# Performance work log

Hardware: AMD Instinct MI355X
Metric: run time of the kernel (lower is better)

## Reference

```python
import jax, jax.numpy as jnp
import numpy as np

NUM_HEADS = 12
ACT_BITS = 8
W_BITS = 8
# I-BERT integer softmax constants (2nd-order polynomial approx of exp on (-ln2, 0])
EXP_COEF = (0.35815147, 0.96963238, 1.0)
LN2 = 0.6931471805599453
N_EXP = 30  # max number of ln2 shifts


def ste_round(x):
    # straight-through round
    return x + jax.lax.stop_gradient(jnp.round(x) - x)


def fq_act(x, bits=ACT_BITS):
    """Per-tensor asymmetric uint fake-quant (QAct). Returns (dequant, scale)."""
    mn = jax.lax.stop_gradient(jnp.min(x))
    mx = jax.lax.stop_gradient(jnp.max(x))
    qmax = 2.0 ** bits - 1.0
    scale = jnp.maximum((mx - mn) / qmax, 1e-8)
    zero = jnp.round(-mn / scale)
    q = jnp.clip(ste_round(x / scale) + zero, 0.0, qmax)
    return (q - zero) * scale, scale


def fq_weight(w, bits=W_BITS):
    """Per-output-channel symmetric int fake-quant (QuantLinear weight)."""
    amax = jax.lax.stop_gradient(jnp.max(jnp.abs(w), axis=1, keepdims=True))
    qmax = 2.0 ** (bits - 1) - 1.0
    scale = jnp.maximum(amax / qmax, 1e-8)
    q = jnp.clip(ste_round(w / scale), -qmax - 1.0, qmax)
    return q * scale


def int_softmax(x, scale):
    """I-BERT style integer softmax; `scale` is the quant scale of x."""
    a, b, c = EXP_COEF
    x_int = ste_round(x / scale)
    x_int = x_int - jnp.max(x_int, axis=-1, keepdims=True)  # <= 0
    x0_int = jnp.floor(-LN2 / scale)                         # negative integer
    x_int = jnp.maximum(x_int, N_EXP * x0_int)
    qexp = jnp.floor(x_int / x0_int)                         # >= 0 integer
    r = x_int - x0_int * qexp                                # residual in (x0_int, 0]
    b_int = jnp.floor(b / a / scale)
    c_int = jnp.floor(c / a / (scale * scale))
    p_int = r * (r + b_int) + c_int                          # int polynomial exp(r)
    e = p_int * jnp.exp2(-qexp) * (a * scale * scale)        # exp(x) approx
    return e / jnp.sum(e, axis=-1, keepdims=True)


def setup_inputs() -> dict:
    key = jax.random.key(0)
    ks = jax.random.split(key, 5)
    B, N, C = 64, 197, 768
    x = jax.random.normal(ks[0], (B, N, C), dtype=jnp.float32)
    w_qkv = jax.random.normal(ks[1], (3 * C, C), dtype=jnp.float32) * 0.02
    b_qkv = jax.random.normal(ks[2], (3 * C,), dtype=jnp.float32) * 0.02
    w_proj = jax.random.normal(ks[3], (C, C), dtype=jnp.float32) * 0.02
    b_proj = jax.random.normal(ks[4], (C,), dtype=jnp.float32) * 0.02
    return {"x": x, "w_qkv": w_qkv, "b_qkv": b_qkv, "w_proj": w_proj, "b_proj": b_proj}


def reference(x, w_qkv, b_qkv, w_proj, b_proj):
    B, N, C = x.shape
    H = NUM_HEADS
    D = C // H
    attn_scale = D ** -0.5

    # QuantLinear qkv: fake-quant weight, GEMM, fake-quant output
    qkv = jnp.einsum('bnc,oc->bno', x, fq_weight(w_qkv)) + b_qkv
    qkv, _ = fq_act(qkv)

    q, _ = fq_act(qkv[:, :, :C])          # attn_q_out
    k, _ = fq_act(qkv[:, :, C:2 * C])     # attn_k_out
    v, _ = fq_act(qkv[:, :, 2 * C:])      # attn_v_input

    q = q.reshape(B, N, H, D).transpose(0, 2, 1, 3)  # bhnd
    k = k.reshape(B, N, H, D).transpose(0, 2, 1, 3)
    v = v.reshape(B, N, H, D).transpose(0, 2, 1, 3)

    attn = jnp.einsum('bhnd,bhmd->bhnm', q, k) * attn_scale
    attn, kv_scale = fq_act(attn)          # attn_kv_out, provides scale to intSoft
    attn = int_softmax(attn, kv_scale)     # QuantIntSoft

    out = jnp.einsum('bhnm,bhmd->bhnd', attn, v)
    out = out.transpose(0, 2, 1, 3).reshape(B, N, C)
    out, _ = fq_act(out)                   # attn_v_out

    out = jnp.einsum('bnc,oc->bno', out, fq_weight(w_proj)) + b_proj
    out, _ = fq_act(out)                   # attn_proj output quant
    return out
```

## Files before the change

### kernel.cpp

```cpp
#include <hip/hip_runtime.h>


#define NB 64
#define NN 197
#define NC 768
#define NH 12
#define ND 64
#define NO3 2304
#define NBH (NB*NH)
#define NM (NB*NN)

typedef unsigned int u32;
typedef unsigned short u16;
typedef unsigned long long u64;
typedef short bf16x8 __attribute__((ext_vector_type(8)));
typedef float f32x4 __attribute__((ext_vector_type(4)));

__device__ __forceinline__ u32 fenc(float f){
  u32 u = __float_as_uint(f);
  return (u & 0x80000000u) ? ~u : (u | 0x80000000u);
}
__device__ __forceinline__ float fdec(u32 e){
  return (e & 0x80000000u) ? __uint_as_float(e ^ 0x80000000u) : __uint_as_float(~e);
}
__device__ __forceinline__ float wmin(float v){
#pragma unroll
  for (int o=32;o>0;o>>=1) v = fminf(v, __shfl_xor(v,o,64));
  return v;
}
__device__ __forceinline__ float wmax(float v){
#pragma unroll
  for (int o=32;o>0;o>>=1) v = fmaxf(v, __shfl_xor(v,o,64));
  return v;
}
__device__ __forceinline__ float fqdq(float x, float s, float z){
  float q = rintf(x/s) + z;
  q = fminf(fmaxf(q, 0.f), 255.f);
  return (q - z) * s;
}
__device__ __forceinline__ u16 tobf(float f){
  u32 u = __float_as_uint(f);
  return (u16)((u + 0x7fffu + ((u >> 16) & 1u)) >> 16);
}
__device__ __forceinline__ float frombf(u16 u){
  return __uint_as_float(((u32)u) << 16);
}

__device__ __forceinline__ void qkv_scales(const u32* slots, float* s2, float* z2,
                                           float* s1o, float* z1o){
  float mnr0=fdec(slots[0]), mxr0=fdec(slots[1]);
  float mnr1=fdec(slots[2]), mxr1=fdec(slots[3]);
  float mnr2=fdec(slots[4]), mxr2=fdec(slots[5]);
  float mn1 = fminf(mnr0, fminf(mnr1, mnr2));
  float mx1 = fmaxf(mxr0, fmaxf(mxr1, mxr2));
  float s1 = fmaxf((mx1-mn1)/255.0f, 1e-8f);
  float z1 = rintf(-mn1/s1);
  float a0 = fqdq(mnr0,s1,z1), b0 = fqdq(mxr0,s1,z1);
  float a1 = fqdq(mnr1,s1,z1), b1 = fqdq(mxr1,s1,z1);
  float a2 = fqdq(mnr2,s1,z1), b2 = fqdq(mxr2,s1,z1);
  s2[0] = fmaxf((b0-a0)/255.0f,1e-8f); z2[0] = rintf(-a0/s2[0]);
  s2[1] = fmaxf((b1-a1)/255.0f,1e-8f); z2[1] = rintf(-a1/s2[1]);
  s2[2] = fmaxf((b2-a2)/255.0f,1e-8f); z2[2] = rintf(-a2/s2[2]);
  *s1o = s1; *z1o = z1;
}

__global__ void k_init(u32* slots){
  int t = threadIdx.x;
  if (t < 12) slots[t] = (t & 1) ? 0u : 0xFFFFFFFFu;
}

__global__ __launch_bounds__(256) void k_wquant(const float* __restrict__ wqkv,
    const float* __restrict__ wproj, u16* __restrict__ B1, float* __restrict__ s1,
    u16* __restrict__ B2, float* __restrict__ s2){
  int row = blockIdx.x;
  const float* src; u16* dst; float* sd;
  if (row < NO3){ src = wqkv + (size_t)row*NC; dst = B1 + (size_t)row*NC; sd = s1 + row; }
  else { int r2 = row - NO3; src = wproj + (size_t)r2*NC; dst = B2 + (size_t)r2*NC; sd = s2 + r2; }
  int t = threadIdx.x;
  float w0 = src[t], w1 = src[t+256], w2 = src[t+512];
  float am = fmaxf(fabsf(w0), fmaxf(fabsf(w1), fabsf(w2)));
  __shared__ float red[4];
  am = wmax(am);
  if ((t&63)==0) red[t>>6] = am;
  __syncthreads();
  am = fmaxf(fmaxf(red[0],red[1]), fmaxf(red[2],red[3]));
  float s = fmaxf(am / 127.0f, 1e-8f);
  dst[t]     = tobf(fminf(fmaxf(rintf(w0/s), -128.f), 127.f));
  dst[t+256] = tobf(fminf(fmaxf(rintf(w1/s), -128.f), 127.f));
  dst[t+512] = tobf(fminf(fmaxf(rintf(w2/s), -128.f), 127.f));
  if (t==0) *sd = s;
}

template<int MODE>
__global__ __launch_bounds__(256) void k_mfma_gemm(const float* __restrict__ A,
    const u16* __restrict__ Bw, const float* __restrict__ sw,
    const float* __restrict__ bias, float* __restrict__ C, int K, int O,
    const u32* __restrict__ qslot, u32* oslot)
{
  __shared__ u16 Ah[128*40];
  __shared__ u16 Al[(MODE==0) ? 128*40 : 8];
  __shared__ u16 Bs[128*40];
  __shared__ float redn[4], redx[4];

  int tid = threadIdx.x;
  int l = tid & 63, w = tid >> 6;
  long m0 = (long)blockIdx.y * 128;
  long o0 = (long)blockIdx.x * 128;
  int srow = tid >> 1;
  int scol = (tid & 1) << 4;
  bool arow_ok = (m0 + srow) < NM;
  const float* Ap = A + (arow_ok ? (m0 + srow) : 0) * (long)K + scol;
  const u16*  Bp = Bw + (o0 + srow) * (long)K + scol;

  float sA = 1.f, zA = 0.f;
  if constexpr (MODE==1){
    float mn = fdec(qslot[0]), mx = fdec(qslot[1]);
    sA = fmaxf((mx-mn)/255.0f, 1e-8f);
    zA = rintf(-mn/sA);
  }

  int wm = (w>>1)*64, wn = (w&1)*64;
  int fr = l & 15;
  int fc = (l>>4)*8;

  f32x4 acc[4][4];
#pragma unroll
  for (int mi=0;mi<4;mi++)
#pragma unroll
    for (int ni=0;ni<4;ni++)
#pragma unroll
      for (int j=0;j<4;j++) acc[mi][ni][j] = 0.f;

  for (int k0=0; k0<K; k0+=32){
    float4 av0, av1, av2, av3;
    if (arow_ok){
      av0 = *(const float4*)(Ap + k0);
      av1 = *(const float4*)(Ap + k0 + 4);
      av2 = *(const float4*)(Ap + k0 + 8);
      av3 = *(const float4*)(Ap + k0 + 12);
    } else {
      av0 = av1 = av2 = av3 = make_float4(0.f,0.f,0.f,0.f);
    }
    uint4 bv0 = *(const uint4*)(Bp + k0);
    uint4 bv1 = *(const uint4*)(Bp + k0 + 8);

    float xs[16];
    *(float4*)&xs[0] = av0; *(float4*)&xs[4]  = av1;
    *(float4*)&xs[8] = av2; *(float4*)&xs[12] = av3;
    bf16x8 h0, h1, lo0, lo1;
    if constexpr (MODE==0){
#pragma unroll
      for (int j=0;j<8;j++){
        u16 h = tobf(xs[j]);
        h0[j]  = (short)h;
        lo0[j] = (short)tobf(xs[j] - frombf(h));
      }
#pragma unroll
      for (int j=0;j<8;j++){
        u16 h = tobf(xs[8+j]);
        h1[j]  = (short)h;
        lo1[j] = (short)tobf(xs[8+j] - frombf(h));
      }
    } else {
#pragma unroll
      for (int j=0;j<16;j++){
        float q = fminf(fmaxf(rintf(xs[j]/sA)+zA, 0.f), 255.f) - zA;
        if (j<8) h0[j] = (short)tobf(q); else h1[j-8] = (short)tobf(q);
      }
    }

    __syncthreads();
    *(bf16x8*)&Ah[srow*40 + scol]     = h0;
    *(bf16x8*)&Ah[srow*40 + scol + 8] = h1;
    if constexpr (MODE==0){
      *(bf16x8*)&Al[srow*40 + scol]     = lo0;
      *(bf16x8*)&Al[srow*40 + scol + 8] = lo1;
    }
    *(bf16x8*)&Bs[srow*40 + scol]     = *(bf16x8*)&bv0;
    *(bf16x8*)&Bs[srow*40 + scol + 8] = *(bf16x8*)&bv1;
    __syncthreads();

    bf16x8 bfr[4];
#pragma unroll
    for (int ni=0;ni<4;ni++)
      bfr[ni] = *(const bf16x8*)&Bs[(wn + ni*16 + fr)*40 + fc];
#pragma unroll
    for (int mi=0;mi<4;mi++){
      bf16x8 ah = *(const bf16x8*)&Ah[(wm + mi*16 + fr)*40 + fc];
#pragma unroll
      for (int ni=0;ni<4;ni++)
        acc[mi][ni] = __builtin_amdgcn_mfma_f32_16x16x32_bf16(ah, bfr[ni], acc[mi][ni], 0, 0, 0);
    }
    if constexpr (MODE==0){
#pragma unroll
      for (int mi=0;mi<4;mi++){
        bf16x8 al = *(const bf16x8*)&Al[(wm + mi*16 + fr)*40 + fc];
#pragma unroll
        for (int ni=0;ni<4;ni++)
          acc[mi][ni] = __builtin_amdgcn_mfma_f32_16x16x32_bf16(al, bfr[ni], acc[mi][ni], 0, 0, 0);
      }
    }
  }

  float cmn = 3.4e38f, cmx = -3.4e38f;
#pragma unroll
  for (int ni=0;ni<4;ni++){
    long col = o0 + wn + ni*16 + fr;
    float sc = sw[col];
    if constexpr (MODE==1) sc *= sA;
    float bb = bias[col];
#pragma unroll
    for (int mi=0;mi<4;mi++){
      long row0 = m0 + wm + mi*16 + (l>>4)*4;
#pragma unroll
      for (int j=0;j<4;j++){
        long rr = row0 + j;
        if (rr < NM){
          float v = acc[mi][ni][j] * sc + bb;
          C[rr*(long)O + col] = v;
          cmn = fminf(cmn, v); cmx = fmaxf(cmx, v);
        }
      }
    }
  }
  cmn = wmin(cmn); cmx = wmax(cmx);
  if (l==0){ redn[w] = cmn; redx[w] = cmx; }
  __syncthreads();
  if (tid==0){
    float mn = fminf(fminf(redn[0],redn[1]), fminf(redn[2],redn[3]));
    float mx = fmaxf(fmaxf(redx[0],redx[1]), fmaxf(redx[2],redx[3]));
    int sb = (MODE==0) ? 2*(int)(blockIdx.x/6) : 0;
    atomicMin(&oslot[sb],   fenc(mn));
    atomicMax(&oslot[sb+1], fenc(mx));
  }
}

__global__ __launch_bounds__(256) void k_transcode(const float* __restrict__ qkv,
    u16* __restrict__ codes, const u32* __restrict__ slots){
  float s2[3], z2[3], s1g, z1g;
  qkv_scales(slots, s2, z2, &s1g, &z1g);
  const u32 total = 3u*NBH*NN*16u;
  for (u32 i4 = blockIdx.x*256u + threadIdx.x; i4 < total; i4 += gridDim.x*256u){
    u32 d4 = i4 & 15u;
    u32 t1 = i4 >> 4;
    u32 n  = t1 % NN;
    u32 t2 = t1 / NN;
    u32 bh = t2 % NBH;
    u32 sl = t2 / NBH;
    u32 b = bh / NH, h = bh % NH;
    float4 v = *(const float4*)(qkv + ((size_t)b*NN + n)*NO3 + sl*NC + h*ND + d4*4u);
    float ss = s2[sl], zz = z2[sl];
    u64 c0 = (u64)tobf(fminf(fmaxf(rintf(fqdq(v.x,s1g,z1g)/ss)+zz,0.f),255.f) - zz);
    u64 c1 = (u64)tobf(fminf(fmaxf(rintf(fqdq(v.y,s1g,z1g)/ss)+zz,0.f),255.f) - zz);
    u64 c2 = (u64)tobf(fminf(fmaxf(rintf(fqdq(v.z,s1g,z1g)/ss)+zz,0.f),255.f) - zz);
    u64 c3 = (u64)tobf(fminf(fmaxf(rintf(fqdq(v.w,s1g,z1g)/ss)+zz,0.f),255.f) - zz);
    *(u64*)(codes + ((size_t)sl*NBH*NN + (size_t)bh*NN + n)*ND + d4*4u) =
        c0 | (c1<<16) | (c2<<32) | (c3<<48);
  }
}

template<int PASS>
__global__ __launch_bounds__(256) void k_attn(const u16* __restrict__ codes,
    float* __restrict__ rowmax, u32* slots, float* __restrict__ outp){
  __shared__ u16 Ks[64*72];
  __shared__ u16 Vt[(PASS==2)?64*72:8];
  __shared__ u16 EsH[(PASS==2)?64*72:8];
  __shared__ u16 EsL[(PASS==2)?64*72:8];
  __shared__ float redn[4], redx[4];

  const u16* qc = codes;
  const u16* kc = codes + (size_t)NBH*NN*ND;
  const u16* vc = codes + 2*(size_t)NBH*NN*ND;

  float s2[3], z2[3], s1g, z1g;
  qkv_scales(slots, s2, z2, &s1g, &z1g);
  float ss = 0.125f * s2[0] * s2[1];
  float sv = s2[2];

  float s=1.f, z=0.f, x0=-1.f, bint=0.f, cint=0.f, as2=0.f, x030=0.f;
  if constexpr (PASS==2){
    float mnA = fdec(slots[6]), mxA = fdec(slots[7]);
    s = fmaxf((mxA-mnA)/255.0f, 1e-8f);
    z = rintf(-mnA/s);
    x0 = floorf(-0.6931471805599453f / s);
    bint = floorf((float)(0.96963238/0.35815147) / s);
    cint = floorf((float)(1.0/0.35815147) / (s*s));
    as2 = (0.35815147f*s)*s;
    x030 = 30.f*x0;
  }

  int tid = threadIdx.x;
  int l = tid & 63, w = tid >> 6;
  int bh = blockIdx.y, nt = blockIdx.x;
  int lr = l & 15, lk = l >> 4;

  int qrow = nt*64 + w*16 + lr;
  bf16x8 aq0 = {}, aq1 = {};
  if (qrow < NN){
    const u16* qp = qc + ((size_t)bh*NN + qrow)*ND + lk*8;
    aq0 = *(const bf16x8*)qp;
    aq1 = *(const bf16x8*)(qp + 32);
  }

  int qr[4];
#pragma unroll
  for (int j=0;j<4;j++) qr[j] = nt*64 + w*16 + lk*4 + j;

  float rcode[4] = {0.f,0.f,0.f,0.f};
  if constexpr (PASS==2){
#pragma unroll
    for (int j=0;j<4;j++)
      if (qr[j] < NN)
        rcode[j] = fminf(fmaxf(rintf(rowmax[(size_t)bh*NN + qr[j]]/s)+z,0.f),255.f);
  }

  float gmn = 3.4e38f, gmx = -3.4e38f;
  float rmx[4] = {-3.4e38f,-3.4e38f,-3.4e38f,-3.4e38f};
  float den[4] = {0.f,0.f,0.f,0.f};
  f32x4 num[4];
#pragma unroll
  for (int dt=0;dt<4;dt++)
#pragma unroll
    for (int j=0;j<4;j++) num[dt][j] = 0.f;

  for (int mt=0; mt<4; mt++){
    __syncthreads();
#pragma unroll
    for (int rep=0; rep<2; rep++){
      int task = tid + rep*256;
      int row = task >> 3, dc = task & 7;
      int grow = mt*64 + row;
      bf16x8 kv8 = {};
      if (grow < NN) kv8 = *(const bf16x8*)(kc + ((size_t)bh*NN + grow)*ND + dc*8);
      *(bf16x8*)&Ks[row*72 + dc*8] = kv8;
      if constexpr (PASS==2){
        bf16x8 vv8 = {};
        if (grow < NN) vv8 = *(const bf16x8*)(vc + ((size_t)bh*NN + grow)*ND + dc*8);
#pragma unroll
        for (int jj=0;jj<8;jj++) Vt[(dc*8+jj)*72 + row] = (u16)vv8[jj];
      }
    }
    __syncthreads();

    f32x4 sca[4];
#pragma unroll
    for (int ct=0;ct<4;ct++)
#pragma unroll
      for (int j=0;j<4;j++) sca[ct][j] = 0.f;
#pragma unroll
    for (int ct=0;ct<4;ct++){
      bf16x8 bk0 = *(const bf16x8*)&Ks[(ct*16 + lr)*72 + lk*8];
      bf16x8 bk1 = *(const bf16x8*)&Ks[(ct*16 + lr)*72 + 32 + lk*8];
      sca[ct] = __builtin_amdgcn_mfma_f32_16x16x32_bf16(aq0, bk0, sca[ct], 0,0,0);
      sca[ct] = __builtin_amdgcn_mfma_f32_16x16x32_bf16(aq1, bk1, sca[ct], 0,0,0);
    }

    if constexpr (PASS==1){
#pragma unroll
      for (int ct=0;ct<4;ct++){
        int m = mt*64 + ct*16 + lr;
        bool mv = m < NN;
#pragma unroll
        for (int j=0;j<4;j++){
          float sc = sca[ct][j] * ss;
          if (mv && qr[j] < NN){
            gmn = fminf(gmn, sc); gmx = fmaxf(gmx, sc);
            rmx[j] = fmaxf(rmx[j], sc);
          }
        }
      }
    } else {
#pragma unroll
      for (int ct=0;ct<4;ct++){
        int m = mt*64 + ct*16 + lr;
        bool mv = m < NN;
#pragma unroll
        for (int j=0;j<4;j++){
          float e = 0.f;
          if (mv && qr[j] < NN){
            float sc = sca[ct][j] * ss;
            float code = fminf(fmaxf(rintf(sc/s)+z, 0.f), 255.f);
            float xx = fmaxf(code - rcode[j], x030);
            float qe = floorf(xx / x0);
            float rr = xx - x0*qe;
            float p = rr*(rr + bint) + cint;
            e = scalbnf(p, -(int)qe) * as2;
            den[j] += e;
          }
          u16 eh = tobf(e);
          int ea = (w*16 + lk*4 + j)*72 + ct*16 + lr;
          EsH[ea] = eh;
          EsL[ea] = tobf(e - frombf(eh));
        }
      }
      __syncthreads();
#pragma unroll
      for (int ks=0; ks<2; ks++){
        bf16x8 ahh = *(const bf16x8*)&EsH[(w*16 + lr)*72 + ks*32 + lk*8];
        bf16x8 ahl = *(const bf16x8*)&EsL[(w*16 + lr)*72 + ks*32 + lk*8];
#pragma unroll
        for (int dt=0; dt<4; dt++){
          bf16x8 bv = *(const bf16x8*)&Vt[(dt*16 + lr)*72 + ks*32 + lk*8];
          num[dt] = __builtin_amdgcn_mfma_f32_16x16x32_bf16(ahh, bv, num[dt], 0,0,0);
          num[dt] = __builtin_amdgcn_mfma_f32_16x16x32_bf16(ahl, bv, num[dt], 0,0,0);
        }
      }
    }
  }

  if constexpr (PASS==1){
#pragma unroll
    for (int j=0;j<4;j++){
#pragma unroll
      for (int o=1;o<16;o<<=1) rmx[j] = fmaxf(rmx[j], __shfl_xor(rmx[j], o, 64));
    }
    if (lr == 0){
#pragma unroll
      for (int j=0;j<4;j++)
        if (qr[j] < NN) rowmax[(size_t)bh*NN + qr[j]] = rmx[j];
    }
    gmn = wmin(gmn); gmx = wmax(gmx);
    if (l==0){ redn[w]=gmn; redx[w]=gmx; }
    __syncthreads();
    if (tid==0){
      float mn = fminf(fminf(redn[0],redn[1]), fminf(redn[2],redn[3]));
      float mx = fmaxf(fmaxf(redx[0],redx[1]), fmaxf(redx[2],redx[3]));
      atomicMin(&slots[6], fenc(mn));
      atomicMax(&slots[7], fenc(mx));
    }
  } else {
#pragma unroll
    for (int j=0;j<4;j++){
#pragma unroll
      for (int o=1;o<16;o<<=1) den[j] += __shfl_xor(den[j], o, 64);
    }
    int b = bh/NH, h = bh - b*NH;
    float gmn2 = 3.4e38f, gmx2 = -3.4e38f;
#pragma unroll
    for (int dt=0;dt<4;dt++){
#pragma unroll
      for (int j=0;j<4;j++){
        if (qr[j] < NN){
          float oo = num[dt][j] * sv / den[j];
          outp[((size_t)b*NN + qr[j])*NC + h*ND + dt*16 + lr] = oo;
          gmn2 = fminf(gmn2, oo); gmx2 = fmaxf(gmx2, oo);
        }
      }
    }
    gmn2 = wmin(gmn2); gmx2 = wmax(gmx2);
    if (l==0){ redn[w]=gmn2; redx[w]=gmx2; }
    __syncthreads();
    if (tid==0){
      float mn = fminf(fminf(redn[0],redn[1]), fminf(redn[2],redn[3]));
      float mx = fmaxf(fmaxf(redx[0],redx[1]), fmaxf(redx[2],redx[3]));
      atomicMin(&slots[8], fenc(mn));
      atomicMax(&slots[9], fenc(mx));
    }
  }
}

__global__ __launch_bounds__(256) void k_fq_inplace(float* x, long n4, const u32* __restrict__ slots){
  float mn = fdec(slots[0]), mx = fdec(slots[1]);
  float s = fmaxf((mx-mn)/255.0f, 1e-8f);
  float z = rintf(-mn/s);
  for (long i = (long)blockIdx.x*blockDim.x + threadIdx.x; i < n4; i += (long)gridDim.x*blockDim.x){
    float4 v = ((float4*)x)[i];
    v.x = fqdq(v.x,s,z); v.y = fqdq(v.y,s,z); v.z = fqdq(v.z,s,z); v.w = fqdq(v.w,s,z);
    ((float4*)x)[i] = v;
  }
}

extern "C" void kernel_launch(void* const* d_in, const int* in_sizes, int n_in,
                              void* d_out, int out_size, void* d_ws, size_t ws_size,
                              hipStream_t stream) {
  (void)in_sizes; (void)n_in; (void)out_size; (void)ws_size;
  const float* x      = (const float*)d_in[0];
  const float* w_qkv  = (const float*)d_in[1];
  const float* b_qkv  = (const float*)d_in[2];
  const float* w_proj = (const float*)d_in[3];
  const float* b_proj = (const float*)d_in[4];
  float* out = (float*)d_out;

  u32*   slots  = (u32*)d_ws;
  u16*   B1     = (u16*)((char*)d_ws + 256);
  u16*   B2     = B1 + (size_t)NO3*NC;
  float* s1     = (float*)(B2 + (size_t)NC*NC);
  float* s2     = s1 + NO3;
  float* rowmax = s2 + NC;
  float* qkv    = rowmax + (size_t)NBH*NN;
  u16*   codes  = (u16*)(qkv + (size_t)NM*NO3);
  float* outpv  = qkv;

  k_init<<<1, 64, 0, stream>>>(slots);
  k_wquant<<<NO3 + NC, 256, 0, stream>>>(w_qkv, w_proj, B1, s1, B2, s2);
  k_mfma_gemm<0><<<dim3(NO3/128, 99), 256, 0, stream>>>(x, B1, s1, b_qkv, qkv, NC, NO3, nullptr, slots);
  k_transcode<<<2048, 256, 0, stream>>>(qkv, codes, slots);
  k_attn<1><<<dim3(4, NBH), 256, 0, stream>>>(codes, rowmax, slots, nullptr);
  k_attn<2><<<dim3(4, NBH), 256, 0, stream>>>(codes, rowmax, slots, outpv);
  k_mfma_gemm<1><<<dim3(NC/128, 99), 256, 0, stream>>>(outpv, B2, s2, b_proj, out, NC, NC, slots + 8, slots + 10);
  k_fq_inplace<<<1024, 256, 0, stream>>>(out, (long)NM*NC/4, slots + 10);
}
```

Baseline: 575.9 us.

## Pre-split GEMM A operands to bf16 and stage tiles with global_load_lds

Moves the fp32-to-bf16 hi/lo split of x and the fake-quant of the attention output into separate pre-pass kernels that write bf16 buffers. The hi and lo halves are laid out as one K=1536 row, so the QKV GEMM runs as a single bf16 GEMM. Both GEMMs now take bf16 A and B tiles with K=64, loaded straight into LDS through global_load_lds, with no per-element conversion in the inner loop. This trades per-iteration conversion ALU work and register staging for extra passes over global memory and two more launches. The unpadded 64-wide LDS rows may cause bank conflicts on the MFMA fragment reads.

```diff
diff --git a/kernel.cpp b/kernel.cpp
--- a/kernel.cpp
+++ b/kernel.cpp
@@ -44,6 +44,11 @@
 }
 __device__ __forceinline__ float frombf(u16 u){
   return __uint_as_float(((u32)u) << 16);
+}
+__device__ __forceinline__ void gload16(const void* g, void* l){
+  __builtin_amdgcn_global_load_lds(
+      (const __attribute__((address_space(1))) void*)g,
+      (__attribute__((address_space(3))) void*)l, 16, 0, 0);
 }
 
 __device__ __forceinline__ void qkv_scales(const u32* slots, float* s2, float* z2,
@@ -91,37 +96,73 @@
   if (t==0) *sd = s;
 }
 
+__global__ __launch_bounds__(256) void k_xsplit(const float* __restrict__ x,
+    u16* __restrict__ xhl){
+  const u32 total = (u32)NM*192u;
+  for (u32 i = blockIdx.x*256u + threadIdx.x; i < total; i += gridDim.x*256u){
+    u32 row = i / 192u, kc = (i - row*192u)*4u;
+    float4 v = *(const float4*)(x + (size_t)row*NC + kc);
+    u16 h0=tobf(v.x), h1=tobf(v.y), h2=tobf(v.z), h3=tobf(v.w);
+    u64 hp = (u64)h0 | ((u64)h1<<16) | ((u64)h2<<32) | ((u64)h3<<48);
+    u64 lp = (u64)tobf(v.x-frombf(h0)) | ((u64)tobf(v.y-frombf(h1))<<16)
+           | ((u64)tobf(v.z-frombf(h2))<<32) | ((u64)tobf(v.w-frombf(h3))<<48);
+    size_t base = (size_t)row*1536 + kc;
+    *(u64*)(xhl + base) = hp;
+    *(u64*)(xhl + base + 768) = lp;
+  }
+}
+
+__global__ __launch_bounds__(256) void k_transcode2(const float* __restrict__ p,
+    u16* __restrict__ codes2, const u32* __restrict__ slots){
+  float mn = fdec(slots[0]), mx = fdec(slots[1]);
+  float s = fmaxf((mx-mn)/255.0f, 1e-8f);
+  float z = rintf(-mn/s);
+  const u32 total = (u32)NM*192u;
+  for (u32 i = blockIdx.x*256u + threadIdx.x; i < total; i += gridDim.x*256u){
+    u32 row = i / 192u, kc = (i - row*192u)*4u;
+    float4 v = *(const float4*)(p + (size_t)row*NC + kc);
+    u64 c0 = (u64)tobf(fminf(fmaxf(rintf(v.x/s)+z,0.f),255.f) - z);
+    u64 c1 = (u64)tobf(fminf(fmaxf(rintf(v.y/s)+z,0.f),255.f) - z);
+    u64 c2 = (u64)tobf(fminf(fmaxf(rintf(v.z/s)+z,0.f),255.f) - z);
+    u64 c3 = (u64)tobf(fminf(fmaxf(rintf(v.w/s)+z,0.f),255.f) - z);
+    *(u64*)(codes2 + (size_t)row*NC + kc) = c0 | (c1<<16) | (c2<<32) | (c3<<48);
+  }
+}
+
 template<int MODE>
-__global__ __launch_bounds__(256) void k_mfma_gemm(const float* __restrict__ A,
+__global__ __launch_bounds__(256) void k_gemm_bf16(const u16* __restrict__ A, int KA,
     const u16* __restrict__ Bw, const float* __restrict__ sw,
-    const float* __restrict__ bias, float* __restrict__ C, int K, int O,
+    const float* __restrict__ bias, float* __restrict__ C, int O,
     const u32* __restrict__ qslot, u32* oslot)
 {
-  __shared__ u16 Ah[128*40];
-  __shared__ u16 Al[(MODE==0) ? 128*40 : 8];
-  __shared__ u16 Bs[128*40];
+  __shared__ u16 As[128*64];
+  __shared__ u16 Bs[128*64];
   __shared__ float redn[4], redx[4];
 
   int tid = threadIdx.x;
   int l = tid & 63, w = tid >> 6;
   long m0 = (long)blockIdx.y * 128;
   long o0 = (long)blockIdx.x * 128;
-  int srow = tid >> 1;
-  int scol = (tid & 1) << 4;
-  bool arow_ok = (m0 + srow) < NM;
-  const float* Ap = A + (arow_ok ? (m0 + srow) : 0) * (long)K + scol;
-  const u16*  Bp = Bw + (o0 + srow) * (long)K + scol;
-
-  float sA = 1.f, zA = 0.f;
+
+  float sA = 1.f;
   if constexpr (MODE==1){
     float mn = fdec(qslot[0]), mx = fdec(qslot[1]);
     sA = fmaxf((mx-mn)/255.0f, 1e-8f);
-    zA = rintf(-mn/sA);
+  }
+
+  int srow = tid >> 3;
+  int scol = (tid & 7) * 8;
+  long arow[4]; const u16* bpr[4];
+#pragma unroll
+  for (int q=0;q<4;q++){
+    long mr = m0 + srow + q*32;
+    arow[q] = (mr < NM) ? mr : (long)(NM-1);
+    bpr[q] = Bw + (size_t)(o0 + srow + q*32) * NC + scol;
   }
 
   int wm = (w>>1)*64, wn = (w&1)*64;
   int fr = l & 15;
-  int fc = (l>>4)*8;
+  int fcb = ((l>>4)*8)*2;
 
   f32x4 acc[4][4];
 #pragma unroll
@@ -131,73 +172,29 @@
 #pragma unroll
       for (int j=0;j<4;j++) acc[mi][ni][j] = 0.f;
 
-  for (int k0=0; k0<K; k0+=32){
-    float4 av0, av1, av2, av3;
-    if (arow_ok){
-      av0 = *(const float4*)(Ap + k0);
-      av1 = *(const float4*)(Ap + k0 + 4);
-      av2 = *(const float4*)(Ap + k0 + 8);
-      av3 = *(const float4*)(Ap + k0 + 12);
-    } else {
-      av0 = av1 = av2 = av3 = make_float4(0.f,0.f,0.f,0.f);
-    }
-    uint4 bv0 = *(const uint4*)(Bp + k0);
-    uint4 bv1 = *(const uint4*)(Bp + k0 + 8);
-
-    float xs[16];
-    *(float4*)&xs[0] = av0; *(float4*)&xs[4]  = av1;
-    *(float4*)&xs[8] = av2; *(float4*)&xs[12] = av3;
-    bf16x8 h0, h1, lo0, lo1;
-    if constexpr (MODE==0){
-#pragma unroll
-      for (int j=0;j<8;j++){
-        u16 h = tobf(xs[j]);
-        h0[j]  = (short)h;
-        lo0[j] = (short)tobf(xs[j] - frombf(h));
-      }
-#pragma unroll
-      for (int j=0;j<8;j++){
-        u16 h = tobf(xs[8+j]);
-        h1[j]  = (short)h;
-        lo1[j] = (short)tobf(xs[8+j] - frombf(h));
-      }
-    } else {
-#pragma unroll
-      for (int j=0;j<16;j++){
-        float q = fminf(fmaxf(rintf(xs[j]/sA)+zA, 0.f), 255.f) - zA;
-        if (j<8) h0[j] = (short)tobf(q); else h1[j-8] = (short)tobf(q);
-      }
-    }
-
+  int nkt = KA >> 6;
+  for (int kt=0; kt<nkt; kt++){
+    int ka0 = kt*64;
+    int kb0 = (ka0 >= NC) ? (ka0 - NC) : ka0;
     __syncthreads();
-    *(bf16x8*)&Ah[srow*40 + scol]     = h0;
-    *(bf16x8*)&Ah[srow*40 + scol + 8] = h1;
-    if constexpr (MODE==0){
-      *(bf16x8*)&Al[srow*40 + scol]     = lo0;
-      *(bf16x8*)&Al[srow*40 + scol + 8] = lo1;
-    }
-    *(bf16x8*)&Bs[srow*40 + scol]     = *(bf16x8*)&bv0;
-    *(bf16x8*)&Bs[srow*40 + scol + 8] = *(bf16x8*)&bv1;
+#pragma unroll
+    for (int q=0;q<4;q++){
+      gload16(A + (size_t)arow[q]*KA + ka0 + scol, &As[(srow + q*32)*64 + scol]);
+      gload16(bpr[q] + kb0,                        &Bs[(srow + q*32)*64 + scol]);
+    }
     __syncthreads();
-
-    bf16x8 bfr[4];
-#pragma unroll
-    for (int ni=0;ni<4;ni++)
-      bfr[ni] = *(const bf16x8*)&Bs[(wn + ni*16 + fr)*40 + fc];
-#pragma unroll
-    for (int mi=0;mi<4;mi++){
-      bf16x8 ah = *(const bf16x8*)&Ah[(wm + mi*16 + fr)*40 + fc];
+#pragma unroll
+    for (int ks=0; ks<2; ks++){
+      bf16x8 bfr[4];
 #pragma unroll
       for (int ni=0;ni<4;ni++)
-        acc[mi][ni] = __builtin_amdgcn_mfma_f32_16x16x32_bf16(ah, bfr[ni], acc[mi][ni], 0, 0, 0);
-    }
-    if constexpr (MODE==0){
+        bfr[ni] = *(const bf16x8*)((const char*)&Bs[(wn + ni*16 + fr)*64] + ks*64 + fcb);
 #pragma unroll
       for (int mi=0;mi<4;mi++){
-        bf16x8 al = *(const bf16x8*)&Al[(wm + mi*16 + fr)*40 + fc];
+        bf16x8 af = *(const bf16x8*)((const char*)&As[(wm + mi*16 + fr)*64] + ks*64 + fcb);
 #pragma unroll
         for (int ni=0;ni<4;ni++)
-          acc[mi][ni] = __builtin_amdgcn_mfma_f32_16x16x32_bf16(al, bfr[ni], acc[mi][ni], 0, 0, 0);
+          acc[mi][ni] = __builtin_amdgcn_mfma_f32_16x16x32_bf16(af, bfr[ni], acc[mi][ni], 0,0,0);
       }
     }
   }
@@ -488,15 +485,20 @@
   float* s2     = s1 + NO3;
   float* rowmax = s2 + NC;
   float* qkv    = rowmax + (size_t)NBH*NN;
-  u16*   codes  = (u16*)(qkv + (size_t)NM*NO3);
+  u16*   codesR = (u16*)(qkv + (size_t)NM*NO3);
+  u16*   xhl    = codesR;
+  u16*   codes  = codesR;
+  u16*   codes2 = codesR;
   float* outpv  = qkv;
 
   k_init<<<1, 64, 0, stream>>>(slots);
   k_wquant<<<NO3 + NC, 256, 0, stream>>>(w_qkv, w_proj, B1, s1, B2, s2);
-  k_mfma_gemm<0><<<dim3(NO3/128, 99), 256, 0, stream>>>(x, B1, s1, b_qkv, qkv, NC, NO3, nullptr, slots);
+  k_xsplit<<<1024, 256, 0, stream>>>(x, xhl);
+  k_gemm_bf16<0><<<dim3(NO3/128, 99), 256, 0, stream>>>(xhl, 1536, B1, s1, b_qkv, qkv, NO3, nullptr, slots);
   k_transcode<<<2048, 256, 0, stream>>>(qkv, codes, slots);
   k_attn<1><<<dim3(4, NBH), 256, 0, stream>>>(codes, rowmax, slots, nullptr);
   k_attn<2><<<dim3(4, NBH), 256, 0, stream>>>(codes, rowmax, slots, outpv);
-  k_mfma_gemm<1><<<dim3(NC/128, 99), 256, 0, stream>>>(outpv, B2, s2, b_proj, out, NC, NC, slots + 8, slots + 10);
+  k_transcode2<<<1024, 256, 0, stream>>>(outpv, codes2, slots + 8);
+  k_gemm_bf16<1><<<dim3(NC/128, 99), 256, 0, stream>>>(codes2, 768, B2, s2, b_proj, out, NC, slots + 8, slots + 10);
   k_fq_inplace<<<1024, 256, 0, stream>>>(out, (long)NM*NC/4, slots + 10);
 }
```

After: 551.3 us. 4.3% less time.
